# Performance work log

Hardware: AMD Instinct MI355X
Metric: run time of the kernel (lower is better)

Reference implementation:

```python
import jax, jax.numpy as jnp
import numpy as np

# Model dims (match init_kwargs)
B, S, D_MODEL = 4, 4096, 2048
D_CACHE = 256
NUM_SLOTS = 128
NUM_LAYERS = 12
LAYER_IDX = 3
D_META = 17  # 1 confidence + 8 layer + 4 iter + 4 pass embeds
D_SLOT = D_CACHE + D_META  # 273
FIXED_THRESH = 0.5
LN_EPS = 1e-5


def setup_inputs() -> dict:
    key = jax.random.key(0)
    ks = jax.random.split(key, 14)
    def lin(k, fan_in, fan_out):
        # xavier-uniform-ish init, stored as [in, out]
        lim = (6.0 / (fan_in + fan_out)) ** 0.5
        return jax.random.uniform(k, (fan_in, fan_out), jnp.float32, -lim, lim)
    inp = {
        "x": jax.random.normal(ks[0], (B, S, D_MODEL), jnp.float32),
        "cache": jax.random.normal(ks[1], (B, NUM_LAYERS * NUM_SLOTS, D_SLOT), jnp.float32),
        # read_gate: LayerNorm(d_model) -> Linear(d_model, d_model//2) -> SiLU -> Linear(d_model//2, 1)
        "ln_w": jnp.ones((D_MODEL,), jnp.float32),
        "ln_b": jnp.zeros((D_MODEL,), jnp.float32),
        "g1_w": lin(ks[2], D_MODEL, D_MODEL // 2),
        "g1_b": jnp.zeros((D_MODEL // 2,), jnp.float32),
        "g2_w": lin(ks[3], D_MODEL // 2, 1),
        "g2_b": jnp.zeros((1,), jnp.float32),
        # read_query: Linear(d_model, d_cache)
        "rq_w": lin(ks[4], D_MODEL, D_CACHE),
        "rq_b": jnp.zeros((D_CACHE,), jnp.float32),
        # from_cache: Linear(d_slot, d_model)
        "fc_w": lin(ks[5], D_SLOT, D_MODEL),
        "fc_b": jnp.zeros((D_MODEL,), jnp.float32),
    }
    return inp


def _layernorm(x, w, b):
    mu = jnp.mean(x, axis=-1, keepdims=True)
    var = jnp.mean(jnp.square(x - mu), axis=-1, keepdims=True)
    return (x - mu) * jax.lax.rsqrt(var + LN_EPS) * w + b


def reference(x, cache, ln_w, ln_b, g1_w, g1_b, g2_w, g2_b, rq_w, rq_b, fc_w, fc_b):
    # ----- read gate (eval mode: hard threshold, no dropout) -----
    h = _layernorm(x, ln_w, ln_b)
    h = jax.nn.silu(h @ g1_w + g1_b)
    gate_logit = h @ g2_w + g2_b                      # [B, S, 1]
    soft_gate = jax.nn.sigmoid(gate_logit)
    read_gate = (soft_gate > FIXED_THRESH).astype(x.dtype)

    # ----- query + local cache slice -----
    query = x @ rq_w + rq_b                           # [B, S, D_cache]
    start = LAYER_IDX * NUM_SLOTS
    local = jax.lax.dynamic_slice_in_dim(cache, start, NUM_SLOTS, axis=1)  # [B, K, D_slot]
    content = local[..., :D_CACHE]                    # [B, K, D_cache]

    # ----- scaled dot-product attention over slots -----
    scores = jnp.einsum("bsd,bkd->bsk", query, content) / np.sqrt(D_CACHE)
    scores = jnp.clip(scores, -20.0, 20.0)
    attn = jax.nn.softmax(scores, axis=-1)            # [B, S, K]
    context_full = jnp.einsum("bsk,bkd->bsd", attn, local)  # retrieve full slot incl. metadata
    context = context_full @ fc_w + fc_b              # [B, S, D_model]

    x_enhanced = x + read_gate * context
    return (x_enhanced, context, attn)
```

## Files before the change

kernel.cpp:

```cpp
#include <hip/hip_runtime.h>
#include <math.h>

#define DM     2048
#define DMH    1024
#define DC     256
#define NSLOT  128
#define DSLOT  273
#define KPAD   288
#define MTOT   16384
#define CROWS  1536
#define SLOT0  384
#define MAXR   4096
#define TAU    2e-3f

typedef __attribute__((ext_vector_type(8))) short  short8;
typedef __attribute__((ext_vector_type(8))) __bf16 bf16x8;
typedef __attribute__((ext_vector_type(4))) float  f32x4;

__device__ inline ushort f2bf(float f) {
    unsigned u = __builtin_bit_cast(unsigned, f);
    unsigned r = (u + 0x7FFFu + ((u >> 16) & 1u)) >> 16;
    return (ushort)r;
}
__device__ inline float bf2f(ushort h) {
    unsigned u = ((unsigned)h) << 16;
    return __builtin_bit_cast(float, u);
}

__global__ __launch_bounds__(256) void k_ln_stats(const float* __restrict__ x,
    float* __restrict__ mu, float* __restrict__ rsig, float* __restrict__ logits,
    int* __restrict__ cnt)
{
    int row = blockIdx.x;
    const float* xr = x + (size_t)row * DM;
    int t = threadIdx.x;
    float4 v0 = *(const float4*)(xr + t * 4);
    float4 v1 = *(const float4*)(xr + 1024 + t * 4);
    float s = v0.x + v0.y + v0.z + v0.w + v1.x + v1.y + v1.z + v1.w;
#pragma unroll
    for (int m = 1; m < 64; m <<= 1) s += __shfl_xor(s, m);
    __shared__ float red[4];
    if ((t & 63) == 0) red[t >> 6] = s;
    __syncthreads();
    float mean = (red[0] + red[1] + red[2] + red[3]) * (1.0f / DM);
    float q = 0.f, d;
    d = v0.x - mean; q += d * d;  d = v0.y - mean; q += d * d;
    d = v0.z - mean; q += d * d;  d = v0.w - mean; q += d * d;
    d = v1.x - mean; q += d * d;  d = v1.y - mean; q += d * d;
    d = v1.z - mean; q += d * d;  d = v1.w - mean; q += d * d;
#pragma unroll
    for (int m = 1; m < 64; m <<= 1) q += __shfl_xor(q, m);
    __syncthreads();
    if ((t & 63) == 0) red[t >> 6] = q;
    __syncthreads();
    float var = (red[0] + red[1] + red[2] + red[3]) * (1.0f / DM);
    if (t == 0) { mu[row] = mean; rsig[row] = rsqrtf(var + 1e-5f); logits[row] = 0.f; }
    if (row == 0 && t == 0) *cnt = 0;
}

__global__ __launch_bounds__(256) void k_prep_w(const float* __restrict__ g1w,
    const float* __restrict__ rqw, const float* __restrict__ fcw,
    ushort* __restrict__ Bh, ushort* __restrict__ Bl,
    ushort* __restrict__ rqwt, ushort* __restrict__ fcwt)
{
    int idx = blockIdx.x * 256 + threadIdx.x;
    {
        int nn = idx >> 11, k = idx & 2047;
        float v = g1w[(size_t)k * DMH + nn];
        ushort h = f2bf(v);
        Bh[idx] = h;
        Bl[idx] = f2bf(v - bf2f(h));
    }
    if (idx < DC * DM) {
        int nn = idx >> 11, k = idx & 2047;
        rqwt[idx] = f2bf(rqw[(size_t)k * DC + nn]);
    }
    if (idx < DM * KPAD) {
        int nn = idx / KPAD, kk = idx - nn * KPAD;
        fcwt[idx] = (kk < DSLOT) ? f2bf(fcw[(size_t)kk * DM + nn]) : (ushort)0;
    }
}

__global__ __launch_bounds__(256) void k_prep_a(const float* __restrict__ x,
    const float* __restrict__ mu, const float* __restrict__ rsig,
    const float* __restrict__ lnw, const float* __restrict__ lnb,
    ushort* __restrict__ Ah, ushort* __restrict__ Al)
{
    int e8 = blockIdx.x * 256 + threadIdx.x;
    int row = e8 >> 8, c = (e8 & 255) * 8;
    float mm = mu[row], rs = rsig[row];
    const float* xp = x + (size_t)row * DM + c;
    float4 a = *(const float4*)xp, b = *(const float4*)(xp + 4);
    float4 w0 = *(const float4*)(lnw + c), w1 = *(const float4*)(lnw + c + 4);
    float4 b0 = *(const float4*)(lnb + c), b1 = *(const float4*)(lnb + c + 4);
    float v[8] = {(a.x-mm)*rs*w0.x+b0.x, (a.y-mm)*rs*w0.y+b0.y,
                  (a.z-mm)*rs*w0.z+b0.z, (a.w-mm)*rs*w0.w+b0.w,
                  (b.x-mm)*rs*w1.x+b1.x, (b.y-mm)*rs*w1.y+b1.y,
                  (b.z-mm)*rs*w1.z+b1.z, (b.w-mm)*rs*w1.w+b1.w};
    ushort h[8]; uint4 oh, ol;
#pragma unroll
    for (int e = 0; e < 8; e++) h[e] = f2bf(v[e]);
    oh.x = h[0] | ((unsigned)h[1] << 16); oh.y = h[2] | ((unsigned)h[3] << 16);
    oh.z = h[4] | ((unsigned)h[5] << 16); oh.w = h[6] | ((unsigned)h[7] << 16);
#pragma unroll
    for (int e = 0; e < 8; e++) h[e] = f2bf(v[e] - bf2f(h[e]));
    ol.x = h[0] | ((unsigned)h[1] << 16); ol.y = h[2] | ((unsigned)h[3] << 16);
    ol.z = h[4] | ((unsigned)h[5] << 16); ol.w = h[6] | ((unsigned)h[7] << 16);
    *(uint4*)(Ah + (size_t)e8 * 8) = oh;
    *(uint4*)(Al + (size_t)e8 * 8) = ol;
}

__global__ __launch_bounds__(256) void k_prep_xh(const float* __restrict__ x, ushort* __restrict__ xh)
{
    int e8 = blockIdx.x * 256 + threadIdx.x;
    const float* xp = x + (size_t)e8 * 8;
    float4 a = *(const float4*)xp, b = *(const float4*)(xp + 4);
    float v[8] = {a.x,a.y,a.z,a.w,b.x,b.y,b.z,b.w};
    ushort h[8]; uint4 o;
#pragma unroll
    for (int e = 0; e < 8; e++) h[e] = f2bf(v[e]);
    o.x = h[0] | ((unsigned)h[1] << 16); o.y = h[2] | ((unsigned)h[3] << 16);
    o.z = h[4] | ((unsigned)h[5] << 16); o.w = h[6] | ((unsigned)h[7] << 16);
    *(uint4*)(xh + (size_t)e8 * 8) = o;
}

template<int MODE>
__global__ __launch_bounds__(256) void k_mfma(
    const ushort* __restrict__ A0, const ushort* __restrict__ A1,
    const ushort* __restrict__ B0, const ushort* __restrict__ B1,
    int K, int N,
    const float* __restrict__ g1b, const float* __restrict__ g2w,
    float* __restrict__ logits,
    const float* __restrict__ bias, float* __restrict__ outc,
    const float* __restrict__ xin, float* __restrict__ outxe,
    const float* __restrict__ g2b)
{
    __shared__ __align__(16) ushort Asl[128 * 32];
    __shared__ __align__(16) ushort Bsl[128 * 32];
    int tid = threadIdx.x;
    int wid = tid >> 6, l = tid & 63;
    int m0 = blockIdx.y * 128, n0 = blockIdx.x * 128;
    int m_off = (wid >> 1) * 64, n_off = (wid & 1) * 64;
    int lr = l & 15, lk = l >> 4;
    int arow = l >> 2, ak8 = (l & 3) * 8;

    f32x4 acc[4][4];
#pragma unroll
    for (int i = 0; i < 4; i++)
#pragma unroll
        for (int j = 0; j < 4; j++) acc[i][j] = (f32x4){0.f, 0.f, 0.f, 0.f};

    const int NSEG = (MODE == 0) ? 3 : 1;
    for (int s = 0; s < NSEG; s++) {
        const ushort* As = (s == 2) ? A1 : A0;
        const ushort* Bs = (s == 1) ? B1 : B0;
        for (int k0 = 0; k0 < K; k0 += 32) {
#pragma unroll
            for (int q = 0; q < 2; q++) {
                int chunk = q * 4 + wid;
                int row = chunk * 16 + arow;
                const ushort* ga = As + (size_t)(m0 + row) * K + k0 + ak8;
                const ushort* gb = Bs + (size_t)(n0 + row) * K + k0 + ak8;
                __builtin_amdgcn_global_load_lds(
                    (const __attribute__((address_space(1))) void*)ga,
                    (__attribute__((address_space(3))) void*)(Asl + chunk * 512), 16, 0, 0);
                __builtin_amdgcn_global_load_lds(
                    (const __attribute__((address_space(1))) void*)gb,
                    (__attribute__((address_space(3))) void*)(Bsl + chunk * 512), 16, 0, 0);
            }
            __syncthreads();
            bf16x8 af[4], bfr[4];
#pragma unroll
            for (int i = 0; i < 4; i++)
                af[i] = __builtin_bit_cast(bf16x8, *(const short8*)&Asl[(m_off + i * 16 + lr) * 32 + lk * 8]);
#pragma unroll
            for (int j = 0; j < 4; j++)
                bfr[j] = __builtin_bit_cast(bf16x8, *(const short8*)&Bsl[(n_off + j * 16 + lr) * 32 + lk * 8]);
#pragma unroll
            for (int i = 0; i < 4; i++)
#pragma unroll
                for (int j = 0; j < 4; j++)
                    acc[i][j] = __builtin_amdgcn_mfma_f32_16x16x32_bf16(af[i], bfr[j], acc[i][j], 0, 0, 0);
            __syncthreads();
        }
    }

    if (MODE == 0) {
        float gb_[4], gw_[4];
#pragma unroll
        for (int j = 0; j < 4; j++) {
            int c = n0 + n_off + j * 16 + lr;
            gb_[j] = g1b[c]; gw_[j] = g2w[c];
        }
#pragma unroll
        for (int i = 0; i < 4; i++)
#pragma unroll
            for (int v = 0; v < 4; v++) {
                float p = 0.f;
#pragma unroll
                for (int j = 0; j < 4; j++) {
                    float h = acc[i][j][v] + gb_[j];
                    p += (h / (1.f + expf(-h))) * gw_[j];
                }
#pragma unroll
                for (int m = 1; m < 16; m <<= 1) p += __shfl_xor(p, m);
                if (lr == 0) atomicAdd(&logits[m0 + m_off + i * 16 + lk * 4 + v], p);
            }
    } else {
        float bias4[4];
#pragma unroll
        for (int j = 0; j < 4; j++) bias4[j] = bias[n0 + n_off + j * 16 + lr];
        float g2b0 = (MODE == 2) ? g2b[0] : 0.f;
#pragma unroll
        for (int i = 0; i < 4; i++)
#pragma unroll
            for (int v = 0; v < 4; v++) {
                int m = m0 + m_off + i * 16 + lk * 4 + v;
                float gt = 0.f;
                if (MODE == 2) gt = (logits[m] + g2b0) > 0.f ? 1.f : 0.f;
#pragma unroll
                for (int j = 0; j < 4; j++) {
                    int c = n0 + n_off + j * 16 + lr;
                    float val = acc[i][j][v] + bias4[j];
                    outc[(size_t)m * N + c] = val;
                    if (MODE == 2) outxe[(size_t)m * DM + c] = xin[(size_t)m * DM + c] + gt * val;
                }
            }
    }
}

__global__ __launch_bounds__(256) void k_compact(float* __restrict__ logits,
    const float* __restrict__ g2b, int* __restrict__ cnt, int* __restrict__ list)
{
    int i = blockIdx.x * 256 + threadIdx.x;
    float a = logits[i] + g2b[0];
    if (fabsf(a) < TAU) {
        int p = atomicAdd(cnt, 1);
        if (p < MAXR) { list[p] = i; logits[i] = 0.f; }
    }
}

__global__ __launch_bounds__(256) void k_refine(const float* __restrict__ x,
    const float* __restrict__ mu, const float* __restrict__ rsig,
    const float* __restrict__ lnw, const float* __restrict__ lnb,
    const float* __restrict__ g1w, const float* __restrict__ g1b,
    const float* __restrict__ g2w,
    const int* __restrict__ list, const int* __restrict__ cnt,
    float* __restrict__ logits)
{
    __shared__ float lnx[DM];
    __shared__ float red[256];
    int tid = threadIdx.x;
    int n = *cnt; if (n > MAXR) n = MAXR;
    int ntask = n * 8;
    for (int t = blockIdx.x; t < ntask; t += gridDim.x) {
        int row = list[t >> 3], sl = t & 7;
        float mm = mu[row], rs = rsig[row];
        {
            int c = tid * 8;
            const float* xp = x + (size_t)row * DM + c;
            float4 a = *(const float4*)xp, b = *(const float4*)(xp + 4);
            float4 w0 = *(const float4*)(lnw + c), w1 = *(const float4*)(lnw + c + 4);
            float4 b0 = *(const float4*)(lnb + c), b1 = *(const float4*)(lnb + c + 4);
            lnx[c+0] = (a.x-mm)*rs*w0.x+b0.x; lnx[c+1] = (a.y-mm)*rs*w0.y+b0.y;
            lnx[c+2] = (a.z-mm)*rs*w0.z+b0.z; lnx[c+3] = (a.w-mm)*rs*w0.w+b0.w;
            lnx[c+4] = (b.x-mm)*rs*w1.x+b1.x; lnx[c+5] = (b.y-mm)*rs*w1.y+b1.y;
            lnx[c+6] = (b.z-mm)*rs*w1.z+b1.z; lnx[c+7] = (b.w-mm)*rs*w1.w+b1.w;
        }
        __syncthreads();
        int j0 = tid & 127, half = tid >> 7;
        int col = sl * 128 + j0;
        const float* gp = g1w + (size_t)(half * 1024) * DMH + col;
        const float* lp = lnx + half * 1024;
        float s = 0.f;
#pragma unroll 4
        for (int k = 0; k < 1024; k++) s += lp[k] * gp[(size_t)k * DMH];
        red[tid] = s;
        __syncthreads();
        if (tid < 128) {
            float h = red[tid] + red[tid + 128] + g1b[col];
            float p = (h / (1.f + expf(-h))) * g2w[col];
#pragma unroll
            for (int m = 1; m < 64; m <<= 1) p += __shfl_xor(p, m);
            red[tid] = p;
        }
        __syncthreads();
        if (tid == 0) atomicAdd(&logits[row], red[0] + red[64]);
        __syncthreads();
    }
}

__global__ __launch_bounds__(256) void k_attn(const float* __restrict__ query,
    const float* __restrict__ cache, float* __restrict__ attn_out, ushort* __restrict__ ctxb)
{
    __shared__ float qs[16][260];
    __shared__ float cs[128][68];
    __shared__ float as_[16][132];
    int tid = threadIdx.x;
    int m0 = blockIdx.x * 16;
    int b = m0 >> 12;
    const size_t cbase = ((size_t)b * CROWS + SLOT0) * DSLOT;

#pragma unroll
    for (int i = 0; i < 4; i++) {
        int f = tid + i * 256;
        int row = f >> 6, c4 = f & 63;
        float4 v = *(const float4*)(query + (size_t)(m0 + row) * DC + c4 * 4);
        *(float4*)&qs[row][c4 * 4] = v;
    }
    int r = tid >> 4, tx = tid & 15;
    float sc[8];
#pragma unroll
    for (int j = 0; j < 8; j++) sc[j] = 0.f;

    for (int d0 = 0; d0 < DC; d0 += 64) {
        __syncthreads();
        for (int idx = tid; idx < 128 * 64; idx += 256) {
            int slot = idx >> 6, dd = idx & 63;
            cs[slot][dd] = cache[cbase + (size_t)slot * DSLOT + d0 + dd];
        }
        __syncthreads();
        for (int dd = 0; dd < 64; dd++) {
            float qv = qs[r][d0 + dd];
#pragma unroll
            for (int j = 0; j < 8; j++) sc[j] += qv * cs[tx + 16 * j][dd];
        }
    }
    float mx = -1e30f;
#pragma unroll
    for (int j = 0; j < 8; j++) {
        sc[j] *= 0.0625f;
        sc[j] = fminf(fmaxf(sc[j], -20.f), 20.f);
        mx = fmaxf(mx, sc[j]);
    }
#pragma unroll
    for (int m = 1; m < 16; m <<= 1) mx = fmaxf(mx, __shfl_xor(mx, m));
    float sum = 0.f;
#pragma unroll
    for (int j = 0; j < 8; j++) { float e = expf(sc[j] - mx); sc[j] = e; sum += e; }
#pragma unroll
    for (int m = 1; m < 16; m <<= 1) sum += __shfl_xor(sum, m);
    float inv = 1.f / sum;
#pragma unroll
    for (int j = 0; j < 8; j++) as_[r][tx + 16 * j] = sc[j] * inv;
    __syncthreads();

#pragma unroll
    for (int i = 0; i < 2; i++) {
        int f = tid + i * 256;
        int row = f >> 5, c4 = f & 31;
        float4 v = *(const float4*)&as_[row][c4 * 4];
        *(float4*)(attn_out + (size_t)(m0 + row) * NSLOT + c4 * 4) = v;
    }

    float* ls = &cs[0][0];
    float ctx[18];
#pragma unroll
    for (int i = 0; i < 18; i++) ctx[i] = 0.f;
    for (int k0 = 0; k0 < NSLOT; k0 += 16) {
        __syncthreads();
        for (int idx = tid; idx < 16 * DSLOT; idx += 256) {
            int kk = idx / DSLOT, c = idx % DSLOT;
            ls[kk * DSLOT + c] = cache[cbase + (size_t)(k0 + kk) * DSLOT + c];
        }
        __syncthreads();
#pragma unroll
        for (int kk = 0; kk < 16; kk++) {
            float a = as_[r][k0 + kk];
#pragma unroll
            for (int i = 0; i < 18; i++) {
                int c = tx + 16 * i;
                if (c < DSLOT) ctx[i] += a * ls[kk * DSLOT + c];
            }
        }
    }
    ushort* crow = ctxb + (size_t)(m0 + r) * KPAD;
#pragma unroll
    for (int i = 0; i < 18; i++) { int c = tx + 16 * i; if (c < DSLOT) crow[c] = f2bf(ctx[i]); }
    if (tx < KPAD - DSLOT) crow[DSLOT + tx] = 0;
}

extern "C" void kernel_launch(void* const* d_in, const int* in_sizes, int n_in,
                              void* d_out, int out_size, void* d_ws, size_t ws_size,
                              hipStream_t stream)
{
    (void)in_sizes; (void)n_in; (void)out_size; (void)ws_size;
    const float* x    = (const float*)d_in[0];
    const float* cache= (const float*)d_in[1];
    const float* lnw  = (const float*)d_in[2];
    const float* lnb  = (const float*)d_in[3];
    const float* g1w  = (const float*)d_in[4];
    const float* g1b  = (const float*)d_in[5];
    const float* g2w  = (const float*)d_in[6];
    const float* g2b  = (const float*)d_in[7];
    const float* rqw  = (const float*)d_in[8];
    const float* rqb  = (const float*)d_in[9];
    const float* fcw  = (const float*)d_in[10];
    const float* fcb  = (const float*)d_in[11];

    float* out   = (float*)d_out;
    float* oxe   = out;
    float* octx  = out + (size_t)MTOT * DM;
    float* oattn = out + (size_t)2 * MTOT * DM;

    float*  ws    = (float*)d_ws;
    float*  mu    = ws;
    float*  rsig  = mu + MTOT;
    float*  logits= rsig + MTOT;
    int*    cnt   = (int*)(logits + MTOT);
    int*    list  = cnt + 16;
    float*  query = (float*)(list + MAXR);
    ushort* ctxb  = (ushort*)(query + (size_t)MTOT * DC);
    ushort* Bh    = ctxb + (size_t)MTOT * KPAD;
    ushort* Bl    = Bh + (size_t)DMH * DM;
    ushort* rqwt  = Bl + (size_t)DMH * DM;
    ushort* fcwt  = rqwt + (size_t)DC * DM;
    ushort* Ah    = fcwt + (size_t)DM * KPAD;
    ushort* Al    = Ah + (size_t)MTOT * DM;

    k_prep_w<<<(DMH * DM) / 256, 256, 0, stream>>>(g1w, rqw, fcw, Bh, Bl, rqwt, fcwt);
    k_ln_stats<<<MTOT, 256, 0, stream>>>(x, mu, rsig, logits, cnt);
    k_prep_a<<<(MTOT * DM / 8) / 256, 256, 0, stream>>>(x, mu, rsig, lnw, lnb, Ah, Al);
    k_mfma<0><<<dim3(DMH / 128, MTOT / 128), 256, 0, stream>>>(Ah, Al, Bh, Bl, DM, DMH,
        g1b, g2w, logits, nullptr, nullptr, nullptr, nullptr, nullptr);
    k_compact<<<MTOT / 256, 256, 0, stream>>>(logits, g2b, cnt, list);
    k_prep_xh<<<(MTOT * DM / 8) / 256, 256, 0, stream>>>(x, Al);
    k_refine<<<512, 256, 0, stream>>>(x, mu, rsig, lnw, lnb, g1w, g1b, g2w, list, cnt, logits);
    k_mfma<1><<<dim3(DC / 128, MTOT / 128), 256, 0, stream>>>(Al, nullptr, rqwt, nullptr, DM, DC,
        nullptr, nullptr, nullptr, rqb, query, nullptr, nullptr, nullptr);
    k_attn<<<MTOT / 16, 256, 0, stream>>>(query, cache, oattn, ctxb);
    k_mfma<2><<<dim3(DM / 128, MTOT / 128), 256, 0, stream>>>(ctxb, nullptr, fcwt, nullptr, KPAD, DM,
        nullptr, nullptr, logits, fcb, octx, x, oxe, g2b);
}
```

Before: 1.205 ms.

## Drop split-bf16 gate GEMM, fuse LN prep, widen refine band, coalesce epilogue

The gate GEMM now runs as a single bf16 pass instead of three hi/lo split passes. To compensate, the fp32 refinement threshold is widened and the list capacity and refine grid are doubled. LayerNorm stats, normalization and the bf16 copy of x are fused into one kernel, removing two full passes over x. The output epilogue is staged through shared memory for coalesced float4 stores, and the attention cache tile load is simplified. The trade-off is less gate precision plus more fp32 refine work, which risks wrong threshold decisions near zero.

```diff
diff --git a/kernel.cpp b/kernel.cpp
--- a/kernel.cpp
+++ b/kernel.cpp
@@ -10,8 +10,8 @@
 #define MTOT   16384
 #define CROWS  1536
 #define SLOT0  384
-#define MAXR   4096
-#define TAU    2e-3f
+#define MAXR   8192
+#define TAU    0.025f
 
 typedef __attribute__((ext_vector_type(8))) short  short8;
 typedef __attribute__((ext_vector_type(8))) __bf16 bf16x8;
@@ -27,49 +27,64 @@
     return __builtin_bit_cast(float, u);
 }
 
-__global__ __launch_bounds__(256) void k_ln_stats(const float* __restrict__ x,
+__global__ __launch_bounds__(256) void k_lnprep(const float* __restrict__ x,
+    const float* __restrict__ lnw, const float* __restrict__ lnb,
     float* __restrict__ mu, float* __restrict__ rsig, float* __restrict__ logits,
-    int* __restrict__ cnt)
+    int* __restrict__ cnt, ushort* __restrict__ Ah, ushort* __restrict__ xh)
 {
     int row = blockIdx.x;
-    const float* xr = x + (size_t)row * DM;
     int t = threadIdx.x;
-    float4 v0 = *(const float4*)(xr + t * 4);
-    float4 v1 = *(const float4*)(xr + 1024 + t * 4);
-    float s = v0.x + v0.y + v0.z + v0.w + v1.x + v1.y + v1.z + v1.w;
+    int c = t * 8;
+    const float* xp = x + (size_t)row * DM + c;
+    float4 a = *(const float4*)xp, b = *(const float4*)(xp + 4);
+    float xr[8] = {a.x, a.y, a.z, a.w, b.x, b.y, b.z, b.w};
+
+    float s = xr[0]+xr[1]+xr[2]+xr[3]+xr[4]+xr[5]+xr[6]+xr[7];
 #pragma unroll
     for (int m = 1; m < 64; m <<= 1) s += __shfl_xor(s, m);
     __shared__ float red[4];
     if ((t & 63) == 0) red[t >> 6] = s;
     __syncthreads();
     float mean = (red[0] + red[1] + red[2] + red[3]) * (1.0f / DM);
-    float q = 0.f, d;
-    d = v0.x - mean; q += d * d;  d = v0.y - mean; q += d * d;
-    d = v0.z - mean; q += d * d;  d = v0.w - mean; q += d * d;
-    d = v1.x - mean; q += d * d;  d = v1.y - mean; q += d * d;
-    d = v1.z - mean; q += d * d;  d = v1.w - mean; q += d * d;
+    float q = 0.f;
+#pragma unroll
+    for (int e = 0; e < 8; e++) { float d = xr[e] - mean; q += d * d; }
 #pragma unroll
     for (int m = 1; m < 64; m <<= 1) q += __shfl_xor(q, m);
     __syncthreads();
     if ((t & 63) == 0) red[t >> 6] = q;
     __syncthreads();
     float var = (red[0] + red[1] + red[2] + red[3]) * (1.0f / DM);
-    if (t == 0) { mu[row] = mean; rsig[row] = rsqrtf(var + 1e-5f); logits[row] = 0.f; }
+    float rs = rsqrtf(var + 1e-5f);
+
+    float4 w0 = *(const float4*)(lnw + c), w1 = *(const float4*)(lnw + c + 4);
+    float4 b0 = *(const float4*)(lnb + c), b1 = *(const float4*)(lnb + c + 4);
+    float wv[8] = {w0.x,w0.y,w0.z,w0.w,w1.x,w1.y,w1.z,w1.w};
+    float bv[8] = {b0.x,b0.y,b0.z,b0.w,b1.x,b1.y,b1.z,b1.w};
+    ushort h[8]; uint4 oh, ox;
+#pragma unroll
+    for (int e = 0; e < 8; e++) h[e] = f2bf((xr[e] - mean) * rs * wv[e] + bv[e]);
+    oh.x = h[0] | ((unsigned)h[1] << 16); oh.y = h[2] | ((unsigned)h[3] << 16);
+    oh.z = h[4] | ((unsigned)h[5] << 16); oh.w = h[6] | ((unsigned)h[7] << 16);
+#pragma unroll
+    for (int e = 0; e < 8; e++) h[e] = f2bf(xr[e]);
+    ox.x = h[0] | ((unsigned)h[1] << 16); ox.y = h[2] | ((unsigned)h[3] << 16);
+    ox.z = h[4] | ((unsigned)h[5] << 16); ox.w = h[6] | ((unsigned)h[7] << 16);
+    size_t base = (size_t)row * DM + c;
+    *(uint4*)(Ah + base) = oh;
+    *(uint4*)(xh + base) = ox;
+    if (t == 0) { mu[row] = mean; rsig[row] = rs; logits[row] = 0.f; }
     if (row == 0 && t == 0) *cnt = 0;
 }
 
 __global__ __launch_bounds__(256) void k_prep_w(const float* __restrict__ g1w,
     const float* __restrict__ rqw, const float* __restrict__ fcw,
-    ushort* __restrict__ Bh, ushort* __restrict__ Bl,
-    ushort* __restrict__ rqwt, ushort* __restrict__ fcwt)
+    ushort* __restrict__ Bh, ushort* __restrict__ rqwt, ushort* __restrict__ fcwt)
 {
     int idx = blockIdx.x * 256 + threadIdx.x;
     {
         int nn = idx >> 11, k = idx & 2047;
-        float v = g1w[(size_t)k * DMH + nn];
-        ushort h = f2bf(v);
-        Bh[idx] = h;
-        Bl[idx] = f2bf(v - bf2f(h));
+        Bh[idx] = f2bf(g1w[(size_t)k * DMH + nn]);
     }
     if (idx < DC * DM) {
         int nn = idx >> 11, k = idx & 2047;
@@ -81,53 +96,9 @@
     }
 }
 
-__global__ __launch_bounds__(256) void k_prep_a(const float* __restrict__ x,
-    const float* __restrict__ mu, const float* __restrict__ rsig,
-    const float* __restrict__ lnw, const float* __restrict__ lnb,
-    ushort* __restrict__ Ah, ushort* __restrict__ Al)
-{
-    int e8 = blockIdx.x * 256 + threadIdx.x;
-    int row = e8 >> 8, c = (e8 & 255) * 8;
-    float mm = mu[row], rs = rsig[row];
-    const float* xp = x + (size_t)row * DM + c;
-    float4 a = *(const float4*)xp, b = *(const float4*)(xp + 4);
-    float4 w0 = *(const float4*)(lnw + c), w1 = *(const float4*)(lnw + c + 4);
-    float4 b0 = *(const float4*)(lnb + c), b1 = *(const float4*)(lnb + c + 4);
-    float v[8] = {(a.x-mm)*rs*w0.x+b0.x, (a.y-mm)*rs*w0.y+b0.y,
-                  (a.z-mm)*rs*w0.z+b0.z, (a.w-mm)*rs*w0.w+b0.w,
-                  (b.x-mm)*rs*w1.x+b1.x, (b.y-mm)*rs*w1.y+b1.y,
-                  (b.z-mm)*rs*w1.z+b1.z, (b.w-mm)*rs*w1.w+b1.w};
-    ushort h[8]; uint4 oh, ol;
-#pragma unroll
-    for (int e = 0; e < 8; e++) h[e] = f2bf(v[e]);
-    oh.x = h[0] | ((unsigned)h[1] << 16); oh.y = h[2] | ((unsigned)h[3] << 16);
-    oh.z = h[4] | ((unsigned)h[5] << 16); oh.w = h[6] | ((unsigned)h[7] << 16);
-#pragma unroll
-    for (int e = 0; e < 8; e++) h[e] = f2bf(v[e] - bf2f(h[e]));
-    ol.x = h[0] | ((unsigned)h[1] << 16); ol.y = h[2] | ((unsigned)h[3] << 16);
-    ol.z = h[4] | ((unsigned)h[5] << 16); ol.w = h[6] | ((unsigned)h[7] << 16);
-    *(uint4*)(Ah + (size_t)e8 * 8) = oh;
-    *(uint4*)(Al + (size_t)e8 * 8) = ol;
-}
-
-__global__ __launch_bounds__(256) void k_prep_xh(const float* __restrict__ x, ushort* __restrict__ xh)
-{
-    int e8 = blockIdx.x * 256 + threadIdx.x;
-    const float* xp = x + (size_t)e8 * 8;
-    float4 a = *(const float4*)xp, b = *(const float4*)(xp + 4);
-    float v[8] = {a.x,a.y,a.z,a.w,b.x,b.y,b.z,b.w};
-    ushort h[8]; uint4 o;
-#pragma unroll
-    for (int e = 0; e < 8; e++) h[e] = f2bf(v[e]);
-    o.x = h[0] | ((unsigned)h[1] << 16); o.y = h[2] | ((unsigned)h[3] << 16);
-    o.z = h[4] | ((unsigned)h[5] << 16); o.w = h[6] | ((unsigned)h[7] << 16);
-    *(uint4*)(xh + (size_t)e8 * 8) = o;
-}
-
 template<int MODE>
 __global__ __launch_bounds__(256) void k_mfma(
-    const ushort* __restrict__ A0, const ushort* __restrict__ A1,
-    const ushort* __restrict__ B0, const ushort* __restrict__ B1,
+    const ushort* __restrict__ A0, const ushort* __restrict__ B0,
     int K, int N,
     const float* __restrict__ g1b, const float* __restrict__ g2w,
     float* __restrict__ logits,
@@ -135,8 +106,9 @@
     const float* __restrict__ xin, float* __restrict__ outxe,
     const float* __restrict__ g2b)
 {
-    __shared__ __align__(16) ushort Asl[128 * 32];
-    __shared__ __align__(16) ushort Bsl[128 * 32];
+    __shared__ __align__(16) ushort smem[8448];
+    ushort* Asl = smem;
+    ushort* Bsl = smem + 4096;
     int tid = threadIdx.x;
     int wid = tid >> 6, l = tid & 63;
     int m0 = blockIdx.y * 128, n0 = blockIdx.x * 128;
@@ -150,39 +122,34 @@
 #pragma unroll
         for (int j = 0; j < 4; j++) acc[i][j] = (f32x4){0.f, 0.f, 0.f, 0.f};
 
-    const int NSEG = (MODE == 0) ? 3 : 1;
-    for (int s = 0; s < NSEG; s++) {
-        const ushort* As = (s == 2) ? A1 : A0;
-        const ushort* Bs = (s == 1) ? B1 : B0;
-        for (int k0 = 0; k0 < K; k0 += 32) {
-#pragma unroll
-            for (int q = 0; q < 2; q++) {
-                int chunk = q * 4 + wid;
-                int row = chunk * 16 + arow;
-                const ushort* ga = As + (size_t)(m0 + row) * K + k0 + ak8;
-                const ushort* gb = Bs + (size_t)(n0 + row) * K + k0 + ak8;
-                __builtin_amdgcn_global_load_lds(
-                    (const __attribute__((address_space(1))) void*)ga,
-                    (__attribute__((address_space(3))) void*)(Asl + chunk * 512), 16, 0, 0);
-                __builtin_amdgcn_global_load_lds(
-                    (const __attribute__((address_space(1))) void*)gb,
-                    (__attribute__((address_space(3))) void*)(Bsl + chunk * 512), 16, 0, 0);
-            }
-            __syncthreads();
-            bf16x8 af[4], bfr[4];
-#pragma unroll
-            for (int i = 0; i < 4; i++)
-                af[i] = __builtin_bit_cast(bf16x8, *(const short8*)&Asl[(m_off + i * 16 + lr) * 32 + lk * 8]);
+    for (int k0 = 0; k0 < K; k0 += 32) {
+#pragma unroll
+        for (int q = 0; q < 2; q++) {
+            int chunk = q * 4 + wid;
+            int row = chunk * 16 + arow;
+            const ushort* ga = A0 + (size_t)(m0 + row) * K + k0 + ak8;
+            const ushort* gb = B0 + (size_t)(n0 + row) * K + k0 + ak8;
+            __builtin_amdgcn_global_load_lds(
+                (const __attribute__((address_space(1))) void*)ga,
+                (__attribute__((address_space(3))) void*)(Asl + chunk * 512), 16, 0, 0);
+            __builtin_amdgcn_global_load_lds(
+                (const __attribute__((address_space(1))) void*)gb,
+                (__attribute__((address_space(3))) void*)(Bsl + chunk * 512), 16, 0, 0);
+        }
+        __syncthreads();
+        bf16x8 af[4], bfr[4];
+#pragma unroll
+        for (int i = 0; i < 4; i++)
+            af[i] = __builtin_bit_cast(bf16x8, *(const short8*)&Asl[(m_off + i * 16 + lr) * 32 + lk * 8]);
+#pragma unroll
+        for (int j = 0; j < 4; j++)
+            bfr[j] = __builtin_bit_cast(bf16x8, *(const short8*)&Bsl[(n_off + j * 16 + lr) * 32 + lk * 8]);
+#pragma unroll
+        for (int i = 0; i < 4; i++)
 #pragma unroll
             for (int j = 0; j < 4; j++)
-                bfr[j] = __builtin_bit_cast(bf16x8, *(const short8*)&Bsl[(n_off + j * 16 + lr) * 32 + lk * 8]);
-#pragma unroll
-            for (int i = 0; i < 4; i++)
-#pragma unroll
-                for (int j = 0; j < 4; j++)
-                    acc[i][j] = __builtin_amdgcn_mfma_f32_16x16x32_bf16(af[i], bfr[j], acc[i][j], 0, 0, 0);
-            __syncthreads();
-        }
+                acc[i][j] = __builtin_amdgcn_mfma_f32_16x16x32_bf16(af[i], bfr[j], acc[i][j], 0, 0, 0);
+        __syncthreads();
     }
 
     if (MODE == 0) {
@@ -207,25 +174,40 @@
                 if (lr == 0) atomicAdd(&logits[m0 + m_off + i * 16 + lk * 4 + v], p);
             }
     } else {
-        float bias4[4];
-#pragma unroll
-        for (int j = 0; j < 4; j++) bias4[j] = bias[n0 + n_off + j * 16 + lr];
+        float* eps = (float*)smem;
         float g2b0 = (MODE == 2) ? g2b[0] : 0.f;
-#pragma unroll
-        for (int i = 0; i < 4; i++)
-#pragma unroll
-            for (int v = 0; v < 4; v++) {
-                int m = m0 + m_off + i * 16 + lk * 4 + v;
-                float gt = 0.f;
-                if (MODE == 2) gt = (logits[m] + g2b0) > 0.f ? 1.f : 0.f;
-#pragma unroll
-                for (int j = 0; j < 4; j++) {
-                    int c = n0 + n_off + j * 16 + lr;
-                    float val = acc[i][j][v] + bias4[j];
-                    outc[(size_t)m * N + c] = val;
-                    if (MODE == 2) outxe[(size_t)m * DM + c] = xin[(size_t)m * DM + c] + gt * val;
+        int rl = (wid >> 1) * 16;
+        int rloc = tid >> 3, c0 = (tid & 7) * 16;
+        float4 bb[4];
+#pragma unroll
+        for (int cc = 0; cc < 4; cc++) bb[cc] = *(const float4*)(bias + n0 + c0 + cc * 4);
+#pragma unroll
+        for (int i = 0; i < 4; i++) {
+            __syncthreads();
+#pragma unroll
+            for (int j = 0; j < 4; j++)
+#pragma unroll
+                for (int v = 0; v < 4; v++)
+                    eps[(rl + lk * 4 + v) * 132 + n_off + j * 16 + lr] = acc[i][j][v];
+            __syncthreads();
+            int m = m0 + (rloc >> 4) * 64 + i * 16 + (rloc & 15);
+            float gt = 0.f;
+            if (MODE == 2) gt = (logits[m] + g2b0) > 0.f ? 1.f : 0.f;
+            float* orow = outc + (size_t)m * N + n0 + c0;
+            const float* xrow = (MODE == 2) ? (xin + (size_t)m * DM + n0 + c0) : nullptr;
+            float* erow = (MODE == 2) ? (outxe + (size_t)m * DM + n0 + c0) : nullptr;
+#pragma unroll
+            for (int cc = 0; cc < 4; cc++) {
+                float4 vv = *(float4*)&eps[rloc * 132 + c0 + cc * 4];
+                vv.x += bb[cc].x; vv.y += bb[cc].y; vv.z += bb[cc].z; vv.w += bb[cc].w;
+                *(float4*)(orow + cc * 4) = vv;
+                if (MODE == 2) {
+                    float4 xv = *(const float4*)(xrow + cc * 4);
+                    float4 ev = {xv.x + gt*vv.x, xv.y + gt*vv.y, xv.z + gt*vv.z, xv.w + gt*vv.w};
+                    *(float4*)(erow + cc * 4) = ev;
                 }
             }
+        }
     }
 }
 
@@ -359,9 +341,11 @@
     for (int i = 0; i < 18; i++) ctx[i] = 0.f;
     for (int k0 = 0; k0 < NSLOT; k0 += 16) {
         __syncthreads();
-        for (int idx = tid; idx < 16 * DSLOT; idx += 256) {
-            int kk = idx / DSLOT, c = idx % DSLOT;
-            ls[kk * DSLOT + c] = cache[cbase + (size_t)(k0 + kk) * DSLOT + c];
+        const float* src = cache + cbase + (size_t)(k0 + r) * DSLOT;
+#pragma unroll
+        for (int i = 0; i < 18; i++) {
+            int c = tx + 16 * i;
+            if (c < DSLOT) ls[r * DSLOT + c] = src[c];
         }
         __syncthreads();
 #pragma unroll
@@ -412,23 +396,20 @@
     float*  query = (float*)(list + MAXR);
     ushort* ctxb  = (ushort*)(query + (size_t)MTOT * DC);
     ushort* Bh    = ctxb + (size_t)MTOT * KPAD;
-    ushort* Bl    = Bh + (size_t)DMH * DM;
-    ushort* rqwt  = Bl + (size_t)DMH * DM;
+    ushort* rqwt  = Bh + (size_t)DMH * DM;
     ushort* fcwt  = rqwt + (size_t)DC * DM;
     ushort* Ah    = fcwt + (size_t)DM * KPAD;
-    ushort* Al    = Ah + (size_t)MTOT * DM;
-
-    k_prep_w<<<(DMH * DM) / 256, 256, 0, stream>>>(g1w, rqw, fcw, Bh, Bl, rqwt, fcwt);
-    k_ln_stats<<<MTOT, 256, 0, stream>>>(x, mu, rsig, logits, cnt);
-    k_prep_a<<<(MTOT * DM / 8) / 256, 256, 0, stream>>>(x, mu, rsig, lnw, lnb, Ah, Al);
-    k_mfma<0><<<dim3(DMH / 128, MTOT / 128), 256, 0, stream>>>(Ah, Al, Bh, Bl, DM, DMH,
+    ushort* xh    = Ah + (size_t)MTOT * DM;
+
+    k_prep_w<<<(DMH * DM) / 256, 256, 0, stream>>>(g1w, rqw, fcw, Bh, rqwt, fcwt);
+    k_lnprep<<<MTOT, 256, 0, stream>>>(x, lnw, lnb, mu, rsig, logits, cnt, Ah, xh);
+    k_mfma<0><<<dim3(DMH / 128, MTOT / 128), 256, 0, stream>>>(Ah, Bh, DM, DMH,
         g1b, g2w, logits, nullptr, nullptr, nullptr, nullptr, nullptr);
     k_compact<<<MTOT / 256, 256, 0, stream>>>(logits, g2b, cnt, list);
-    k_prep_xh<<<(MTOT * DM / 8) / 256, 256, 0, stream>>>(x, Al);
-    k_refine<<<512, 256, 0, stream>>>(x, mu, rsig, lnw, lnb, g1w, g1b, g2w, list, cnt, logits);
-    k_mfma<1><<<dim3(DC / 128, MTOT / 128), 256, 0, stream>>>(Al, nullptr, rqwt, nullptr, DM, DC,
+    k_refine<<<1024, 256, 0, stream>>>(x, mu, rsig, lnw, lnb, g1w, g1b, g2w, list, cnt, logits);
+    k_mfma<1><<<dim3(DC / 128, MTOT / 128), 256, 0, stream>>>(xh, rqwt, DM, DC,
         nullptr, nullptr, nullptr, rqb, query, nullptr, nullptr, nullptr);
     k_attn<<<MTOT / 16, 256, 0, stream>>>(query, cache, oattn, ctxb);
-    k_mfma<2><<<dim3(DM / 128, MTOT / 128), 256, 0, stream>>>(ctxb, nullptr, fcwt, nullptr, KPAD, DM,
+    k_mfma<2><<<dim3(DM / 128, MTOT / 128), 256, 0, stream>>>(ctxb, fcwt, KPAD, DM,
         nullptr, nullptr, logits, fcb, octx, x, oxe, g2b);
 }
```

Result: faster. 1.052 ms (-12.7%).
